# Kernel tuning notes

Hardware: AMD Instinct MI355X
Metric: run time of the kernel (lower is better)

The kernel has to match this reference:

```python
import jax, jax.numpy as jnp
import numpy as np

N_NODES = 20000
N_EDGES = 320000
NFEAT = 128
NHID = 64
NCLASS = 16
HEADS = 4
NLAYERS = 3
DT = 1.0
EPS = 1e-5
NEG_SLOPE = 0.2
# softplus(1.0) for Ks, omega, zeta (raw values all 1.0, non-learnable)
SP1 = float(np.log1p(np.exp(1.0)))


def rms_norm(x):
    rms = jnp.sqrt(jnp.mean(x * x, axis=-1, keepdims=True) + EPS)
    return x / rms


def gat_conv(x, src, dst, W_gat, att_src, att_dst, b_gat):
    # x: [N, NHID] -> per-head projections h: [N, H, NHID]
    h = (x @ W_gat).reshape(N_NODES, HEADS, NHID)
    a_src = jnp.sum(h * att_src[None], axis=-1)  # [N, H]
    a_dst = jnp.sum(h * att_dst[None], axis=-1)  # [N, H]
    e = jax.nn.leaky_relu(a_src[src] + a_dst[dst], NEG_SLOPE)  # [E, H]
    # segment softmax over incoming edges of each destination node
    e_max = jax.ops.segment_max(e, dst, num_segments=N_NODES)
    e_max = jnp.where(jnp.isfinite(e_max), e_max, 0.0)
    ex = jnp.exp(e - e_max[dst])
    denom = jax.ops.segment_sum(ex, dst, num_segments=N_NODES)
    alpha = ex / (denom[dst] + 1e-16)  # [E, H]
    msg = h[src] * alpha[:, :, None]  # [E, H, NHID]
    out = jax.ops.segment_sum(msg, dst, num_segments=N_NODES)  # [N, H, NHID]
    return out.reshape(N_NODES, HEADS * NHID) + b_gat


def setup_inputs() -> dict:
    key = jax.random.key(0)
    ks = jax.random.split(key, 10)
    s = 0.05
    x = jax.random.normal(ks[0], (N_NODES, NFEAT), dtype=jnp.float32)
    edge_index = jax.random.randint(ks[1], (2, N_EDGES), 0, N_NODES, dtype=jnp.int64)
    return {
        "x": x,
        "edge_index": edge_index,
        "W_enc": jax.random.normal(ks[2], (NFEAT, NHID), dtype=jnp.float32) * s,
        "b_enc": jnp.zeros((NHID,), dtype=jnp.float32),
        "W_gat": jax.random.normal(ks[3], (NHID, HEADS * NHID), dtype=jnp.float32) * s,
        "att_src": jax.random.normal(ks[4], (HEADS, NHID), dtype=jnp.float32) * s,
        "att_dst": jax.random.normal(ks[5], (HEADS, NHID), dtype=jnp.float32) * s,
        "b_gat": jnp.zeros((HEADS * NHID,), dtype=jnp.float32),
        "W_dec": jax.random.normal(ks[6], (NHID, NCLASS), dtype=jnp.float32) * s,
        "b_dec": jnp.zeros((NCLASS,), dtype=jnp.float32),
    }


def reference(x, edge_index, W_enc, b_enc, W_gat, att_src, att_dst, b_gat, W_dec, b_dec):
    # eval mode: dropout is identity
    Ks, omega, zeta = SP1, SP1, SP1
    omega_sq = omega * omega
    # PyG GATConv add_self_loops=True
    loops = jnp.arange(N_NODES, dtype=edge_index.dtype)
    src = jnp.concatenate([edge_index[0], loops])
    dst = jnp.concatenate([edge_index[1], loops])

    Y = jax.nn.relu(x @ W_enc + b_enc)
    X = Y
    for _ in range(NLAYERS):
        conv = jax.nn.elu(gat_conv(X, src, dst, W_gat, att_src, att_dst, b_gat))
        # faithful to original: view(N, -1, heads).mean(-1) on [N, heads*nhid]
        agg = conv.reshape(N_NODES, NHID, HEADS).mean(axis=-1)
        Y = Y + DT * (Ks * agg - 2.0 * zeta * omega * Y - omega_sq * X)
        X = X + DT * Y
        X = rms_norm(X)
        Y = rms_norm(Y)
    return X @ W_dec + b_dec
```

## Files before the change

kernel.cpp:

```cpp
#include <hip/hip_runtime.h>
#include <hip/hip_bf16.h>

#define DEV static __device__ __forceinline__

constexpr int N_NODES = 20000;
constexpr int N_EDGES = 320000;
constexpr int NFEAT = 128;
constexpr int NHID = 64;
constexpr int NCLASS = 16;
constexpr int HEADS = 4;
constexpr int HD = HEADS * NHID;
constexpr float EPSV = 1e-5f;
constexpr float SLOPE = 0.2f;
constexpr float SP1 = 1.3132616875182228f;

typedef __attribute__((ext_vector_type(8))) short short8;
typedef __attribute__((ext_vector_type(4))) float float4v;

DEV float bf2f(__hip_bfloat16 v) { return __bfloat162float(v); }
DEV short f2bfbits(float v) { return (short)__bfloat16_as_ushort(__float2bfloat16(v)); }
DEV float lrelu(float v) { return v > 0.f ? v : SLOPE * v; }
DEV int clampn(int v) { return min(max(v, 0), N_NODES - 1); }

DEV float ldf(const void* p, int i, int f32) {
  return f32 ? ((const float*)p)[i] : bf2f(((const __hip_bfloat16*)p)[i]);
}
DEV int eload(const int* e32, int is64, int idx) {
  if (is64) return (int)(((const long long*)e32)[idx]);
  return e32[idx];
}

DEV float wsum(float v) {
#pragma unroll
  for (int m = 32; m > 0; m >>= 1) v += __shfl_xor(v, m, 64);
  return v;
}
DEV float qsum(float v) {
#pragma unroll
  for (int m = 1; m < 16; m <<= 1) v += __shfl_xor(v, m, 64);
  return v;
}
DEV void acc8_i8(float* acc, int lo, int hi, float a) {
  acc[0] = fmaf((float)(signed char)(lo), a, acc[0]);
  acc[1] = fmaf((float)(signed char)(lo >> 8), a, acc[1]);
  acc[2] = fmaf((float)(signed char)(lo >> 16), a, acc[2]);
  acc[3] = fmaf((float)(lo >> 24), a, acc[3]);
  acc[4] = fmaf((float)(signed char)(hi), a, acc[4]);
  acc[5] = fmaf((float)(signed char)(hi >> 8), a, acc[5]);
  acc[6] = fmaf((float)(signed char)(hi >> 16), a, acc[6]);
  acc[7] = fmaf((float)(hi >> 24), a, acc[7]);
}

__global__ __launch_bounds__(256) void k_detect_pack(const int* __restrict__ edge,
                                                     const unsigned* __restrict__ xw,
                                                     const void* __restrict__ W_enc,
                                                     const void* __restrict__ W_gat,
                                                     int* __restrict__ flag,
                                                     short* __restrict__ packE,
                                                     short* __restrict__ packG) {
  __shared__ int sflag[2];
  int tid = threadIdx.x;
  if (tid < 64) {
    int v = edge[2 * tid + 1];
    unsigned long long nz = __ballot(v != 0);
    int bad = 0;
#pragma unroll
    for (int j = 0; j < 4; ++j) {
      unsigned w = xw[tid * 4 + j];
      unsigned ex = ((w & 0xFFFFu) >> 7) & 0xFFu;
      if (ex >= 0x90u) bad = 1;
    }
    unsigned long long anybad = __ballot(bad != 0);
    if (tid == 0) {
      sflag[0] = (nz == 0ULL) ? 1 : 0;
      sflag[1] = (anybad != 0ULL) ? 1 : 0;
      flag[0] = sflag[0];
      flag[1] = sflag[1];
    }
  }
  __syncthreads();
  int f32 = sflag[1];
  int wv = tid >> 6, lane = tid & 63;
  int quad = lane >> 4, m16 = lane & 15;
#pragma unroll
  for (int ks = 0; ks < 4; ++ks)
#pragma unroll
    for (int j = 0; j < 8; ++j)
      packE[(ks * 256 + tid) * 8 + j] =
          f2bfbits(ldf(W_enc, (ks * 32 + quad * 8 + j) * NHID + wv * 16 + m16, f32));
#pragma unroll
  for (int t = 0; t < 4; ++t)
#pragma unroll
    for (int ks = 0; ks < 2; ++ks)
#pragma unroll
      for (int j = 0; j < 8; ++j)
        packG[((t * 2 + ks) * 256 + tid) * 8 + j] =
            f2bfbits(ldf(W_gat, (ks * 32 + quad * 8 + j) * HD + wv * 64 + t * 16 + m16, f32));
}

__global__ void k_hist(const int* __restrict__ edge, const int* __restrict__ flag,
                       int* __restrict__ counts) {
  int e = blockIdx.x * blockDim.x + threadIdx.x;
  if (e < N_EDGES) {
    int d = clampn(eload(edge, flag[0], N_EDGES + e));
    atomicAdd(&counts[d], 1);
  }
}

__global__ __launch_bounds__(1024) void k_scan(const int* __restrict__ counts,
                                               int* __restrict__ rowptr,
                                               int* __restrict__ cursor) {
  __shared__ int part[1024];
  int t = threadIdx.x;
  const int CH = (N_NODES + 1023) / 1024;
  int b = t * CH, e = min(b + CH, N_NODES);
  int s = 0;
  for (int i = b; i < e; ++i) s += counts[i];
  part[t] = s;
  __syncthreads();
  for (int off = 1; off < 1024; off <<= 1) {
    int v = (t >= off) ? part[t - off] : 0;
    __syncthreads();
    part[t] += v;
    __syncthreads();
  }
  int run = (t == 0) ? 0 : part[t - 1];
  for (int i = b; i < e; ++i) {
    rowptr[i] = run;
    cursor[i] = run;
    run += counts[i];
  }
  if (t == 1023) rowptr[N_NODES] = N_EDGES;
}

__global__ void k_scatter(const int* __restrict__ edge, const int* __restrict__ flag,
                          int* __restrict__ cursor, int* __restrict__ ssort) {
  int e = blockIdx.x * blockDim.x + threadIdx.x;
  if (e < N_EDGES) {
    int is64 = flag[0];
    int s = clampn(eload(edge, is64, e));
    int d = clampn(eload(edge, is64, N_EDGES + e));
    int pos = atomicAdd(&cursor[d], 1);
    if (pos >= 0 && pos < N_EDGES) ssort[pos] = s;
  }
}

__global__ __launch_bounds__(256) void k_encoder(const void* __restrict__ x,
                                                 const short* __restrict__ packE,
                                                 const void* __restrict__ b_enc,
                                                 const int* __restrict__ flag,
                                                 float* __restrict__ X, float* __restrict__ Y) {
  int f32 = flag[1];
  int tid = threadIdx.x;
  int wv = tid >> 6, lane = tid & 63;
  int quad = lane >> 4, m16 = lane & 15;
  int n0 = blockIdx.x * 16;
  int c0 = wv * 16;

  float4v acc = {0.f, 0.f, 0.f, 0.f};
#pragma unroll
  for (int ks = 0; ks < 4; ++ks) {
    short8 bfrag = *(const short8*)(packE + (ks * 256 + tid) * 8);
    short8 afrag;
    size_t xoff = (size_t)(n0 + m16) * NFEAT + ks * 32 + quad * 8;
    if (f32) {
      float4 f0 = *(const float4*)((const float*)x + xoff);
      float4 f1 = *(const float4*)((const float*)x + xoff + 4);
      afrag[0] = f2bfbits(f0.x); afrag[1] = f2bfbits(f0.y);
      afrag[2] = f2bfbits(f0.z); afrag[3] = f2bfbits(f0.w);
      afrag[4] = f2bfbits(f1.x); afrag[5] = f2bfbits(f1.y);
      afrag[6] = f2bfbits(f1.z); afrag[7] = f2bfbits(f1.w);
    } else {
      afrag = *(const short8*)((const short*)x + xoff);
    }
    acc = __builtin_amdgcn_mfma_f32_16x16x32_bf16(afrag, bfrag, acc, 0, 0, 0);
  }

  float bias = ldf(b_enc, c0 + m16, f32);
#pragma unroll
  for (int r = 0; r < 4; ++r) {
    int n = n0 + quad * 4 + r;
    float yv = fmaxf(acc[r] + bias, 0.f);
    size_t idx = (size_t)n * NHID + c0 + m16;
    X[idx] = yv;
    Y[idx] = yv;
  }
}

__global__ __launch_bounds__(256) void k_proj(const float* __restrict__ X,
                                              const short* __restrict__ packG,
                                              const void* __restrict__ att_src,
                                              const void* __restrict__ att_dst,
                                              const int* __restrict__ flag,
                                              signed char* __restrict__ hb,
                                              float* __restrict__ nodeinfo,
                                              float* __restrict__ a_dst) {
  __shared__ float smax[4][16];
  int f32 = flag[1];
  int tid = threadIdx.x;
  int wv = tid >> 6, lane = tid & 63;
  int quad = lane >> 4, m16 = lane & 15;
  int n0 = blockIdx.x * 16;

  short8 afrag[2];
#pragma unroll
  for (int ks = 0; ks < 2; ++ks) {
    size_t xoff = (size_t)(n0 + m16) * NHID + ks * 32 + quad * 8;
    float4 f0 = *(const float4*)(X + xoff);
    float4 f1 = *(const float4*)(X + xoff + 4);
    afrag[ks][0] = f2bfbits(f0.x); afrag[ks][1] = f2bfbits(f0.y);
    afrag[ks][2] = f2bfbits(f0.z); afrag[ks][3] = f2bfbits(f0.w);
    afrag[ks][4] = f2bfbits(f1.x); afrag[ks][5] = f2bfbits(f1.y);
    afrag[ks][6] = f2bfbits(f1.z); afrag[ks][7] = f2bfbits(f1.w);
  }

  float4v acc[4];
#pragma unroll
  for (int t = 0; t < 4; ++t) {
    acc[t] = (float4v){0.f, 0.f, 0.f, 0.f};
#pragma unroll
    for (int ks = 0; ks < 2; ++ks) {
      short8 bfrag = *(const short8*)(packG + ((t * 2 + ks) * 256 + tid) * 8);
      acc[t] = __builtin_amdgcn_mfma_f32_16x16x32_bf16(afrag[ks], bfrag, acc[t], 0, 0, 0);
    }
  }

  float amax[4];
#pragma unroll
  for (int r = 0; r < 4; ++r) {
    float m = fmaxf(fmaxf(fabsf(acc[0][r]), fabsf(acc[1][r])),
                    fmaxf(fabsf(acc[2][r]), fabsf(acc[3][r])));
#pragma unroll
    for (int sh = 1; sh < 16; sh <<= 1) m = fmaxf(m, __shfl_xor(m, sh, 64));
    amax[r] = m;
  }
  if (m16 == 0) {
#pragma unroll
    for (int r = 0; r < 4; ++r) smax[wv][quad * 4 + r] = amax[r];
  }
  __syncthreads();
  float inv[4], rmax[4];
#pragma unroll
  for (int r = 0; r < 4; ++r) {
    int row = quad * 4 + r;
    float m = fmaxf(fmaxf(smax[0][row], smax[1][row]), fmaxf(smax[2][row], smax[3][row]));
    rmax[r] = m;
    inv[r] = (m > 0.f) ? 127.f / m : 0.f;
  }

  float avs[4], avd[4];
#pragma unroll
  for (int t = 0; t < 4; ++t) {
    avs[t] = ldf(att_src, wv * 64 + t * 16 + m16, f32);
    avd[t] = ldf(att_dst, wv * 64 + t * 16 + m16, f32);
  }
  float ps[4], pd[4];
#pragma unroll
  for (int r = 0; r < 4; ++r) { ps[r] = 0.f; pd[r] = 0.f; }
#pragma unroll
  for (int t = 0; t < 4; ++t) {
#pragma unroll
    for (int r = 0; r < 4; ++r) {
      int n = n0 + quad * 4 + r;
      hb[(size_t)n * HD + wv * 64 + t * 16 + m16] =
          (signed char)__float2int_rn(acc[t][r] * inv[r]);
      ps[r] = fmaf(acc[t][r], avs[t], ps[r]);
      pd[r] = fmaf(acc[t][r], avd[t], pd[r]);
    }
  }
#pragma unroll
  for (int r = 0; r < 4; ++r) {
    float s = qsum(ps[r]);
    float dq = qsum(pd[r]);
    if (m16 == 0) {
      int n = n0 + quad * 4 + r;
      nodeinfo[(size_t)n * 8 + wv * 2] = s;
      nodeinfo[(size_t)n * 8 + wv * 2 + 1] = rmax[r] * (1.f / 127.f);
      a_dst[n * HEADS + wv] = dq;
    }
  }
}

__global__ __launch_bounds__(256) void k_layer(const signed char* __restrict__ hb,
                                               const float* __restrict__ nodeinfo,
                                               const float* __restrict__ a_dst,
                                               const int* __restrict__ rowptr,
                                               const int* __restrict__ srcs,
                                               const void* __restrict__ b_gat,
                                               const int* __restrict__ flag,
                                               float* __restrict__ X, float* __restrict__ Y) {
  int wave = threadIdx.x >> 6, lane = threadIdx.x & 63;
  int half = lane >> 5, l32 = lane & 31, head = l32 >> 3;
  int f32 = flag[1];
  int d = blockIdx.x * 4 + wave;
  if (d >= N_NODES) return;
  int beg = rowptr[d];
  int end = rowptr[d + 1];
  beg = min(max(beg, 0), N_EDGES);
  end = min(max(end, beg), N_EDGES);
  float advh = a_dst[d * 4 + head];

  float acc[8];
#pragma unroll
  for (int k = 0; k < 8; ++k) acc[k] = 0.f;
  float sw = 0.f;

  {
    float2 nid = *(const float2*)(nodeinfo + (size_t)d * 8 + head * 2);
    float wself = __expf(lrelu(nid.x + advh));
    if (half == 0) {
      sw = wself;
      uint2 hv = *(const uint2*)(hb + (size_t)d * HD + l32 * 8);
      acc8_i8(acc, (int)hv.x, (int)hv.y, wself * nid.y);
    }
  }
  int p = beg;
  for (; p + 8 <= end; p += 8) {
    int q0 = p + half, q1 = p + 2 + half, q2 = p + 4 + half, q3 = p + 6 + half;
    int s0 = clampn(srcs[q0]), s1 = clampn(srcs[q1]);
    int s2 = clampn(srcs[q2]), s3 = clampn(srcs[q3]);
    float2 n0v = *(const float2*)(nodeinfo + (size_t)s0 * 8 + head * 2);
    float2 n1v = *(const float2*)(nodeinfo + (size_t)s1 * 8 + head * 2);
    float2 n2v = *(const float2*)(nodeinfo + (size_t)s2 * 8 + head * 2);
    float2 n3v = *(const float2*)(nodeinfo + (size_t)s3 * 8 + head * 2);
    uint2 h0 = *(const uint2*)(hb + (size_t)s0 * HD + l32 * 8);
    uint2 h1 = *(const uint2*)(hb + (size_t)s1 * HD + l32 * 8);
    uint2 h2 = *(const uint2*)(hb + (size_t)s2 * HD + l32 * 8);
    uint2 h3 = *(const uint2*)(hb + (size_t)s3 * HD + l32 * 8);
    float w0 = __expf(lrelu(n0v.x + advh));
    float w1 = __expf(lrelu(n1v.x + advh));
    float w2 = __expf(lrelu(n2v.x + advh));
    float w3 = __expf(lrelu(n3v.x + advh));
    sw += w0 + w1 + w2 + w3;
    acc8_i8(acc, (int)h0.x, (int)h0.y, w0 * n0v.y);
    acc8_i8(acc, (int)h1.x, (int)h1.y, w1 * n1v.y);
    acc8_i8(acc, (int)h2.x, (int)h2.y, w2 * n2v.y);
    acc8_i8(acc, (int)h3.x, (int)h3.y, w3 * n3v.y);
  }
  for (; p < end; p += 2) {
    int q = p + half;
    bool act = q < end;
    int s = clampn(srcs[act ? q : end - 1]);
    float2 nv = *(const float2*)(nodeinfo + (size_t)s * 8 + head * 2);
    uint2 hv = *(const uint2*)(hb + (size_t)s * HD + l32 * 8);
    float w = act ? __expf(lrelu(nv.x + advh)) : 0.f;
    sw += w;
    acc8_i8(acc, (int)hv.x, (int)hv.y, w * nv.y);
  }
  sw += __shfl_xor(sw, 32, 64);
#pragma unroll
  for (int k = 0; k < 8; ++k) acc[k] += __shfl_xor(acc[k], 32, 64);
  float invh = 1.f / (sw + 1e-16f);

  float cg[8];
#pragma unroll
  for (int k = 0; k < 8; ++k) {
    float c = acc[k] * invh + ldf(b_gat, l32 * 8 + k, f32);
    cg[k] = c > 0.f ? c : expm1f(c);
  }
  float agg0 = 0.25f * (cg[0] + cg[1] + cg[2] + cg[3]);
  float agg1 = 0.25f * (cg[4] + cg[5] + cg[6] + cg[7]);

  size_t ix = (size_t)d * NHID + l32 * 2;
  float xv0 = X[ix], xv1 = X[ix + 1];
  float yv0 = Y[ix], yv1 = Y[ix + 1];
  float yn0 = yv0 + (SP1 * agg0 - 2.f * SP1 * SP1 * yv0 - SP1 * SP1 * xv0);
  float yn1 = yv1 + (SP1 * agg1 - 2.f * SP1 * SP1 * yv1 - SP1 * SP1 * xv1);
  float xn0 = xv0 + yn0;
  float xn1 = xv1 + yn1;

  float msx = wsum(xn0 * xn0 + xn1 * xn1) * (1.f / 128.f);
  float rx = rsqrtf(msx + EPSV);
  float msy = wsum(yn0 * yn0 + yn1 * yn1) * (1.f / 128.f);
  float ry = rsqrtf(msy + EPSV);
  X[ix] = xn0 * rx; X[ix + 1] = xn1 * rx;
  Y[ix] = yn0 * ry; Y[ix + 1] = yn1 * ry;
}

__global__ __launch_bounds__(256) void k_dec(const float* __restrict__ X,
                                             const void* __restrict__ W_dec,
                                             const void* __restrict__ b_dec,
                                             const int* __restrict__ flag,
                                             float* __restrict__ out) {
  __shared__ float Wl[NHID * NCLASS];
  __shared__ float bl[NCLASS];
  int f32 = flag[1];
  int tid = threadIdx.x;
  for (int i = tid; i < NHID * NCLASS; i += 256) Wl[i] = ldf(W_dec, i, f32);
  if (tid < NCLASS) bl[tid] = ldf(b_dec, tid, f32);
  __syncthreads();
  int g = blockIdx.x * 256 + tid;
  if (g >= N_NODES * NCLASS) return;
  int n = g >> 4, c = g & 15;
  const float* xr = X + (size_t)n * NHID;
  float acc = bl[c];
#pragma unroll
  for (int k = 0; k < NHID; ++k) acc = fmaf(xr[k], Wl[k * NCLASS + c], acc);
  if (!(acc == acc) || fabsf(acc) > 1e6f) acc = 777.0f;
  out[g] = acc;
}

extern "C" void kernel_launch(void* const* d_in, const int* in_sizes, int n_in,
                              void* d_out, int out_size, void* d_ws, size_t ws_size,
                              hipStream_t stream) {
  const void* x       = d_in[0];
  const int*  edge    = (const int*)d_in[1];
  const void* W_enc   = d_in[2];
  const void* b_enc   = d_in[3];
  const void* W_gat   = d_in[4];
  const void* att_src = d_in[5];
  const void* att_dst = d_in[6];
  const void* b_gat   = d_in[7];
  const void* W_dec   = d_in[8];
  const void* b_dec   = d_in[9];

  char* ws = (char*)d_ws;
  size_t off = 0;
  auto alloc = [&](size_t bytes) -> void* {
    if (off + bytes > ws_size) off = 0;
    void* p = ws + off;
    off = (off + bytes + 255) & ~(size_t)255;
    return p;
  };
  int*   flag    = (int*)alloc(256);
  int*   counts  = (int*)alloc((size_t)N_NODES * 4);
  int*   rowptr  = (int*)alloc((size_t)(N_NODES + 1) * 4);
  int*   cursor  = (int*)alloc((size_t)N_NODES * 4);
  int*   ssort   = (int*)alloc((size_t)N_EDGES * 4);
  float* nodeinfo= (float*)alloc((size_t)N_NODES * 8 * 4);
  float* a_dst   = (float*)alloc((size_t)N_NODES * HEADS * 4);
  float* X       = (float*)alloc((size_t)N_NODES * NHID * 4);
  float* Y       = (float*)alloc((size_t)N_NODES * NHID * 4);
  short* packE   = (short*)alloc((size_t)4 * 256 * 8 * 2);
  short* packG   = (short*)alloc((size_t)8 * 256 * 8 * 2);
  signed char* hb = (signed char*)alloc((size_t)N_NODES * HD);

  hipMemsetAsync(counts, 0, (size_t)N_NODES * 4, stream);
  k_detect_pack<<<1, 256, 0, stream>>>(edge, (const unsigned*)x, W_enc, W_gat, flag, packE, packG);
  k_hist<<<(N_EDGES + 255) / 256, 256, 0, stream>>>(edge, flag, counts);
  k_scan<<<1, 1024, 0, stream>>>(counts, rowptr, cursor);
  k_scatter<<<(N_EDGES + 255) / 256, 256, 0, stream>>>(edge, flag, cursor, ssort);

  k_encoder<<<N_NODES / 16, 256, 0, stream>>>(x, packE, b_enc, flag, X, Y);
  for (int l = 0; l < 3; ++l) {
    k_proj<<<N_NODES / 16, 256, 0, stream>>>(X, packG, att_src, att_dst, flag, hb, nodeinfo, a_dst);
    k_layer<<<N_NODES / 4, 256, 0, stream>>>(hb, nodeinfo, a_dst, rowptr, ssort, b_gat, flag, X, Y);
  }
  k_dec<<<(N_NODES * NCLASS + 255) / 256, 256, 0, stream>>>(X, W_dec, b_dec, flag, (float*)d_out);
}
```

Before: 334.0 us.

## Gather 16 int8 features per lane and process four edges per wave step

```diff
diff --git a/kernel.cpp b/kernel.cpp
--- a/kernel.cpp
+++ b/kernel.cpp
@@ -40,15 +40,17 @@
   for (int m = 1; m < 16; m <<= 1) v += __shfl_xor(v, m, 64);
   return v;
 }
-DEV void acc8_i8(float* acc, int lo, int hi, float a) {
-  acc[0] = fmaf((float)(signed char)(lo), a, acc[0]);
-  acc[1] = fmaf((float)(signed char)(lo >> 8), a, acc[1]);
-  acc[2] = fmaf((float)(signed char)(lo >> 16), a, acc[2]);
-  acc[3] = fmaf((float)(lo >> 24), a, acc[3]);
-  acc[4] = fmaf((float)(signed char)(hi), a, acc[4]);
-  acc[5] = fmaf((float)(signed char)(hi >> 8), a, acc[5]);
-  acc[6] = fmaf((float)(signed char)(hi >> 16), a, acc[6]);
-  acc[7] = fmaf((float)(hi >> 24), a, acc[7]);
+DEV void acc4_i8(float* acc, int w, float a) {
+  acc[0] = fmaf((float)(signed char)(w), a, acc[0]);
+  acc[1] = fmaf((float)(signed char)(w >> 8), a, acc[1]);
+  acc[2] = fmaf((float)(signed char)(w >> 16), a, acc[2]);
+  acc[3] = fmaf((float)(w >> 24), a, acc[3]);
+}
+DEV void acc16_i8(float* acc, uint4 hv, float a) {
+  acc4_i8(acc + 0, (int)hv.x, a);
+  acc4_i8(acc + 4, (int)hv.y, a);
+  acc4_i8(acc + 8, (int)hv.z, a);
+  acc4_i8(acc + 12, (int)hv.w, a);
 }
 
 __global__ __launch_bounds__(256) void k_detect_pack(const int* __restrict__ edge,
@@ -290,7 +292,7 @@
                                                const int* __restrict__ flag,
                                                float* __restrict__ X, float* __restrict__ Y) {
   int wave = threadIdx.x >> 6, lane = threadIdx.x & 63;
-  int half = lane >> 5, l32 = lane & 31, head = l32 >> 3;
+  int qtr = lane >> 4, l16 = lane & 15, head = l16 >> 2;
   int f32 = flag[1];
   int d = blockIdx.x * 4 + wave;
   if (d >= N_NODES) return;
@@ -300,81 +302,82 @@
   end = min(max(end, beg), N_EDGES);
   float advh = a_dst[d * 4 + head];
 
-  float acc[8];
-#pragma unroll
-  for (int k = 0; k < 8; ++k) acc[k] = 0.f;
+  float acc[16];
+#pragma unroll
+  for (int k = 0; k < 16; ++k) acc[k] = 0.f;
   float sw = 0.f;
 
   {
-    float2 nid = *(const float2*)(nodeinfo + (size_t)d * 8 + head * 2);
+    float2 nid = *(const float2*)(nodeinfo + ((unsigned)d << 3) + head * 2);
     float wself = __expf(lrelu(nid.x + advh));
-    if (half == 0) {
+    if (qtr == 0) {
       sw = wself;
-      uint2 hv = *(const uint2*)(hb + (size_t)d * HD + l32 * 8);
-      acc8_i8(acc, (int)hv.x, (int)hv.y, wself * nid.y);
+      uint4 hv = *(const uint4*)(hb + ((unsigned)d << 8) + (l16 << 4));
+      acc16_i8(acc, hv, wself * nid.y);
     }
   }
   int p = beg;
   for (; p + 8 <= end; p += 8) {
-    int q0 = p + half, q1 = p + 2 + half, q2 = p + 4 + half, q3 = p + 6 + half;
-    int s0 = clampn(srcs[q0]), s1 = clampn(srcs[q1]);
-    int s2 = clampn(srcs[q2]), s3 = clampn(srcs[q3]);
-    float2 n0v = *(const float2*)(nodeinfo + (size_t)s0 * 8 + head * 2);
-    float2 n1v = *(const float2*)(nodeinfo + (size_t)s1 * 8 + head * 2);
-    float2 n2v = *(const float2*)(nodeinfo + (size_t)s2 * 8 + head * 2);
-    float2 n3v = *(const float2*)(nodeinfo + (size_t)s3 * 8 + head * 2);
-    uint2 h0 = *(const uint2*)(hb + (size_t)s0 * HD + l32 * 8);
-    uint2 h1 = *(const uint2*)(hb + (size_t)s1 * HD + l32 * 8);
-    uint2 h2 = *(const uint2*)(hb + (size_t)s2 * HD + l32 * 8);
-    uint2 h3 = *(const uint2*)(hb + (size_t)s3 * HD + l32 * 8);
+    int q0 = p + qtr, q1 = p + 4 + qtr;
+    int s0 = srcs[q0], s1 = srcs[q1];
+    float2 n0v = *(const float2*)(nodeinfo + ((unsigned)s0 << 3) + head * 2);
+    float2 n1v = *(const float2*)(nodeinfo + ((unsigned)s1 << 3) + head * 2);
+    uint4 h0 = *(const uint4*)(hb + ((unsigned)s0 << 8) + (l16 << 4));
+    uint4 h1 = *(const uint4*)(hb + ((unsigned)s1 << 8) + (l16 << 4));
     float w0 = __expf(lrelu(n0v.x + advh));
     float w1 = __expf(lrelu(n1v.x + advh));
-    float w2 = __expf(lrelu(n2v.x + advh));
-    float w3 = __expf(lrelu(n3v.x + advh));
-    sw += w0 + w1 + w2 + w3;
-    acc8_i8(acc, (int)h0.x, (int)h0.y, w0 * n0v.y);
-    acc8_i8(acc, (int)h1.x, (int)h1.y, w1 * n1v.y);
-    acc8_i8(acc, (int)h2.x, (int)h2.y, w2 * n2v.y);
-    acc8_i8(acc, (int)h3.x, (int)h3.y, w3 * n3v.y);
-  }
-  for (; p < end; p += 2) {
-    int q = p + half;
+    sw += w0 + w1;
+    acc16_i8(acc, h0, w0 * n0v.y);
+    acc16_i8(acc, h1, w1 * n1v.y);
+  }
+  for (; p < end; p += 4) {
+    int q = p + qtr;
     bool act = q < end;
-    int s = clampn(srcs[act ? q : end - 1]);
-    float2 nv = *(const float2*)(nodeinfo + (size_t)s * 8 + head * 2);
-    uint2 hv = *(const uint2*)(hb + (size_t)s * HD + l32 * 8);
+    int s = act ? srcs[q] : d;
+    float2 nv = *(const float2*)(nodeinfo + ((unsigned)s << 3) + head * 2);
+    uint4 hv = *(const uint4*)(hb + ((unsigned)s << 8) + (l16 << 4));
     float w = act ? __expf(lrelu(nv.x + advh)) : 0.f;
     sw += w;
-    acc8_i8(acc, (int)hv.x, (int)hv.y, w * nv.y);
-  }
+    acc16_i8(acc, hv, w * nv.y);
+  }
+  sw += __shfl_xor(sw, 16, 64);
   sw += __shfl_xor(sw, 32, 64);
 #pragma unroll
-  for (int k = 0; k < 8; ++k) acc[k] += __shfl_xor(acc[k], 32, 64);
+  for (int k = 0; k < 16; ++k) {
+    acc[k] += __shfl_xor(acc[k], 16, 64);
+    acc[k] += __shfl_xor(acc[k], 32, 64);
+  }
   float invh = 1.f / (sw + 1e-16f);
 
-  float cg[8];
-#pragma unroll
-  for (int k = 0; k < 8; ++k) {
-    float c = acc[k] * invh + ldf(b_gat, l32 * 8 + k, f32);
+  float cg[16];
+#pragma unroll
+  for (int k = 0; k < 16; ++k) {
+    float c = acc[k] * invh + ldf(b_gat, l16 * 16 + k, f32);
     cg[k] = c > 0.f ? c : expm1f(c);
   }
-  float agg0 = 0.25f * (cg[0] + cg[1] + cg[2] + cg[3]);
-  float agg1 = 0.25f * (cg[4] + cg[5] + cg[6] + cg[7]);
-
-  size_t ix = (size_t)d * NHID + l32 * 2;
-  float xv0 = X[ix], xv1 = X[ix + 1];
-  float yv0 = Y[ix], yv1 = Y[ix + 1];
-  float yn0 = yv0 + (SP1 * agg0 - 2.f * SP1 * SP1 * yv0 - SP1 * SP1 * xv0);
-  float yn1 = yv1 + (SP1 * agg1 - 2.f * SP1 * SP1 * yv1 - SP1 * SP1 * xv1);
-  float xn0 = xv0 + yn0;
-  float xn1 = xv1 + yn1;
-
-  float msx = wsum(xn0 * xn0 + xn1 * xn1) * (1.f / 128.f);
+  float agg[4];
+#pragma unroll
+  for (int g = 0; g < 4; ++g)
+    agg[g] = 0.25f * (cg[g * 4] + cg[g * 4 + 1] + cg[g * 4 + 2] + cg[g * 4 + 3]);
+
+  size_t ix = (size_t)d * NHID + l16 * 4;
+  float4 xv = *(const float4*)(X + ix);
+  float4 yv = *(const float4*)(Y + ix);
+  float yn[4], xn[4];
+  float xvv[4] = {xv.x, xv.y, xv.z, xv.w};
+  float yvv[4] = {yv.x, yv.y, yv.z, yv.w};
+#pragma unroll
+  for (int g = 0; g < 4; ++g) {
+    yn[g] = yvv[g] + (SP1 * agg[g] - 2.f * SP1 * SP1 * yvv[g] - SP1 * SP1 * xvv[g]);
+    xn[g] = xvv[g] + yn[g];
+  }
+
+  float msx = wsum(xn[0] * xn[0] + xn[1] * xn[1] + xn[2] * xn[2] + xn[3] * xn[3]) * (1.f / 256.f);
   float rx = rsqrtf(msx + EPSV);
-  float msy = wsum(yn0 * yn0 + yn1 * yn1) * (1.f / 128.f);
+  float msy = wsum(yn[0] * yn[0] + yn[1] * yn[1] + yn[2] * yn[2] + yn[3] * yn[3]) * (1.f / 256.f);
   float ry = rsqrtf(msy + EPSV);
-  X[ix] = xn0 * rx; X[ix + 1] = xn1 * rx;
-  Y[ix] = yn0 * ry; Y[ix + 1] = yn1 * ry;
+  *(float4*)(X + ix) = make_float4(xn[0] * rx, xn[1] * rx, xn[2] * rx, xn[3] * rx);
+  *(float4*)(Y + ix) = make_float4(yn[0] * ry, yn[1] * ry, yn[2] * ry, yn[3] * ry);
 }
 
 __global__ __launch_bounds__(256) void k_dec(const float* __restrict__ X,
```

Measured after the change: 392.7 us. +17.6%, slower.

## Merge setup kernels and fuse decoder into last GAT layer

Applied to the files above, without the earlier changes.

```diff
diff --git a/kernel.cpp b/kernel.cpp
--- a/kernel.cpp
+++ b/kernel.cpp
@@ -51,15 +51,28 @@
   acc[7] = fmaf((float)(hi >> 24), a, acc[7]);
 }
 
-__global__ __launch_bounds__(256) void k_detect_pack(const int* __restrict__ edge,
-                                                     const unsigned* __restrict__ xw,
-                                                     const void* __restrict__ W_enc,
-                                                     const void* __restrict__ W_gat,
-                                                     int* __restrict__ flag,
-                                                     short* __restrict__ packE,
-                                                     short* __restrict__ packG) {
+__global__ __launch_bounds__(256) void k_histpack(const int* __restrict__ edge,
+                                                  const unsigned* __restrict__ xw,
+                                                  const void* __restrict__ W_enc,
+                                                  const void* __restrict__ W_gat,
+                                                  int* __restrict__ flag,
+                                                  short* __restrict__ packE,
+                                                  short* __restrict__ packG,
+                                                  int* __restrict__ counts) {
+  int b = blockIdx.x;
+  int tid = threadIdx.x;
+  if (b < 1250) {
+    int lane = tid & 63;
+    int v = edge[2 * lane + 1];
+    int is64 = (__ballot(v != 0) == 0ULL) ? 1 : 0;
+    int e = b * 256 + tid;
+    if (e < N_EDGES) {
+      int d = clampn(eload(edge, is64, N_EDGES + e));
+      atomicAdd(&counts[d], 1);
+    }
+    return;
+  }
   __shared__ int sflag[2];
-  int tid = threadIdx.x;
   if (tid < 64) {
     int v = edge[2 * tid + 1];
     unsigned long long nz = __ballot(v != 0);
@@ -96,15 +109,6 @@
       for (int j = 0; j < 8; ++j)
         packG[((t * 2 + ks) * 256 + tid) * 8 + j] =
             f2bfbits(ldf(W_gat, (ks * 32 + quad * 8 + j) * HD + wv * 64 + t * 16 + m16, f32));
-}
-
-__global__ void k_hist(const int* __restrict__ edge, const int* __restrict__ flag,
-                       int* __restrict__ counts) {
-  int e = blockIdx.x * blockDim.x + threadIdx.x;
-  if (e < N_EDGES) {
-    int d = clampn(eload(edge, flag[0], N_EDGES + e));
-    atomicAdd(&counts[d], 1);
-  }
 }
 
 __global__ __launch_bounds__(1024) void k_scan(const int* __restrict__ counts,
@@ -133,28 +137,32 @@
   if (t == 1023) rowptr[N_NODES] = N_EDGES;
 }
 
-__global__ void k_scatter(const int* __restrict__ edge, const int* __restrict__ flag,
-                          int* __restrict__ cursor, int* __restrict__ ssort) {
-  int e = blockIdx.x * blockDim.x + threadIdx.x;
-  if (e < N_EDGES) {
-    int is64 = flag[0];
-    int s = clampn(eload(edge, is64, e));
-    int d = clampn(eload(edge, is64, N_EDGES + e));
-    int pos = atomicAdd(&cursor[d], 1);
-    if (pos >= 0 && pos < N_EDGES) ssort[pos] = s;
-  }
-}
-
-__global__ __launch_bounds__(256) void k_encoder(const void* __restrict__ x,
-                                                 const short* __restrict__ packE,
-                                                 const void* __restrict__ b_enc,
-                                                 const int* __restrict__ flag,
-                                                 float* __restrict__ X, float* __restrict__ Y) {
+__global__ __launch_bounds__(256) void k_encscatter(const void* __restrict__ x,
+                                                    const short* __restrict__ packE,
+                                                    const void* __restrict__ b_enc,
+                                                    const int* __restrict__ edge,
+                                                    const int* __restrict__ flag,
+                                                    int* __restrict__ cursor,
+                                                    int* __restrict__ ssort,
+                                                    float* __restrict__ X,
+                                                    float* __restrict__ Y) {
+  int blk = blockIdx.x;
+  int tid = threadIdx.x;
+  if (blk >= 1250) {
+    int e = (blk - 1250) * 256 + tid;
+    if (e < N_EDGES) {
+      int is64 = flag[0];
+      int s = clampn(eload(edge, is64, e));
+      int d = clampn(eload(edge, is64, N_EDGES + e));
+      int pos = atomicAdd(&cursor[d], 1);
+      if (pos >= 0 && pos < N_EDGES) ssort[pos] = s;
+    }
+    return;
+  }
   int f32 = flag[1];
-  int tid = threadIdx.x;
   int wv = tid >> 6, lane = tid & 63;
   int quad = lane >> 4, m16 = lane & 15;
-  int n0 = blockIdx.x * 16;
+  int n0 = blk * 16;
   int c0 = wv * 16;
 
   float4v acc = {0.f, 0.f, 0.f, 0.f};
@@ -288,12 +296,15 @@
                                                const int* __restrict__ srcs,
                                                const void* __restrict__ b_gat,
                                                const int* __restrict__ flag,
-                                               float* __restrict__ X, float* __restrict__ Y) {
+                                               float* __restrict__ X, float* __restrict__ Y,
+                                               const void* __restrict__ W_dec,
+                                               const void* __restrict__ b_dec,
+                                               float* __restrict__ out) {
+  __shared__ float xl[4 * NHID];
   int wave = threadIdx.x >> 6, lane = threadIdx.x & 63;
   int half = lane >> 5, l32 = lane & 31, head = l32 >> 3;
   int f32 = flag[1];
   int d = blockIdx.x * 4 + wave;
-  if (d >= N_NODES) return;
   int beg = rowptr[d];
   int end = rowptr[d + 1];
   beg = min(max(beg, 0), N_EDGES);
@@ -306,27 +317,27 @@
   float sw = 0.f;
 
   {
-    float2 nid = *(const float2*)(nodeinfo + (size_t)d * 8 + head * 2);
+    float2 nid = *(const float2*)(nodeinfo + ((unsigned)d << 3) + head * 2);
     float wself = __expf(lrelu(nid.x + advh));
     if (half == 0) {
       sw = wself;
-      uint2 hv = *(const uint2*)(hb + (size_t)d * HD + l32 * 8);
+      uint2 hv = *(const uint2*)(hb + ((unsigned)d << 8) + (l32 << 3));
       acc8_i8(acc, (int)hv.x, (int)hv.y, wself * nid.y);
     }
   }
   int p = beg;
   for (; p + 8 <= end; p += 8) {
     int q0 = p + half, q1 = p + 2 + half, q2 = p + 4 + half, q3 = p + 6 + half;
-    int s0 = clampn(srcs[q0]), s1 = clampn(srcs[q1]);
-    int s2 = clampn(srcs[q2]), s3 = clampn(srcs[q3]);
-    float2 n0v = *(const float2*)(nodeinfo + (size_t)s0 * 8 + head * 2);
-    float2 n1v = *(const float2*)(nodeinfo + (size_t)s1 * 8 + head * 2);
-    float2 n2v = *(const float2*)(nodeinfo + (size_t)s2 * 8 + head * 2);
-    float2 n3v = *(const float2*)(nodeinfo + (size_t)s3 * 8 + head * 2);
-    uint2 h0 = *(const uint2*)(hb + (size_t)s0 * HD + l32 * 8);
-    uint2 h1 = *(const uint2*)(hb + (size_t)s1 * HD + l32 * 8);
-    uint2 h2 = *(const uint2*)(hb + (size_t)s2 * HD + l32 * 8);
-    uint2 h3 = *(const uint2*)(hb + (size_t)s3 * HD + l32 * 8);
+    int s0 = srcs[q0], s1 = srcs[q1];
+    int s2 = srcs[q2], s3 = srcs[q3];
+    float2 n0v = *(const float2*)(nodeinfo + ((unsigned)s0 << 3) + head * 2);
+    float2 n1v = *(const float2*)(nodeinfo + ((unsigned)s1 << 3) + head * 2);
+    float2 n2v = *(const float2*)(nodeinfo + ((unsigned)s2 << 3) + head * 2);
+    float2 n3v = *(const float2*)(nodeinfo + ((unsigned)s3 << 3) + head * 2);
+    uint2 h0 = *(const uint2*)(hb + ((unsigned)s0 << 8) + (l32 << 3));
+    uint2 h1 = *(const uint2*)(hb + ((unsigned)s1 << 8) + (l32 << 3));
+    uint2 h2 = *(const uint2*)(hb + ((unsigned)s2 << 8) + (l32 << 3));
+    uint2 h3 = *(const uint2*)(hb + ((unsigned)s3 << 8) + (l32 << 3));
     float w0 = __expf(lrelu(n0v.x + advh));
     float w1 = __expf(lrelu(n1v.x + advh));
     float w2 = __expf(lrelu(n2v.x + advh));
@@ -340,9 +351,9 @@
   for (; p < end; p += 2) {
     int q = p + half;
     bool act = q < end;
-    int s = clampn(srcs[act ? q : end - 1]);
-    float2 nv = *(const float2*)(nodeinfo + (size_t)s * 8 + head * 2);
-    uint2 hv = *(const uint2*)(hb + (size_t)s * HD + l32 * 8);
+    int s = act ? srcs[q] : d;
+    float2 nv = *(const float2*)(nodeinfo + ((unsigned)s << 3) + head * 2);
+    uint2 hv = *(const uint2*)(hb + ((unsigned)s << 8) + (l32 << 3));
     float w = act ? __expf(lrelu(nv.x + advh)) : 0.f;
     sw += w;
     acc8_i8(acc, (int)hv.x, (int)hv.y, w * nv.y);
@@ -373,31 +384,27 @@
   float rx = rsqrtf(msx + EPSV);
   float msy = wsum(yn0 * yn0 + yn1 * yn1) * (1.f / 128.f);
   float ry = rsqrtf(msy + EPSV);
-  X[ix] = xn0 * rx; X[ix + 1] = xn1 * rx;
+  float fx0 = xn0 * rx, fx1 = xn1 * rx;
+  X[ix] = fx0; X[ix + 1] = fx1;
   Y[ix] = yn0 * ry; Y[ix + 1] = yn1 * ry;
-}
-
-__global__ __launch_bounds__(256) void k_dec(const float* __restrict__ X,
-                                             const void* __restrict__ W_dec,
-                                             const void* __restrict__ b_dec,
-                                             const int* __restrict__ flag,
-                                             float* __restrict__ out) {
-  __shared__ float Wl[NHID * NCLASS];
-  __shared__ float bl[NCLASS];
-  int f32 = flag[1];
-  int tid = threadIdx.x;
-  for (int i = tid; i < NHID * NCLASS; i += 256) Wl[i] = ldf(W_dec, i, f32);
-  if (tid < NCLASS) bl[tid] = ldf(b_dec, tid, f32);
-  __syncthreads();
-  int g = blockIdx.x * 256 + tid;
-  if (g >= N_NODES * NCLASS) return;
-  int n = g >> 4, c = g & 15;
-  const float* xr = X + (size_t)n * NHID;
-  float acc = bl[c];
-#pragma unroll
-  for (int k = 0; k < NHID; ++k) acc = fmaf(xr[k], Wl[k * NCLASS + c], acc);
-  if (!(acc == acc) || fabsf(acc) > 1e6f) acc = 777.0f;
-  out[g] = acc;
+
+  if (out != nullptr) {
+    if (half == 0) {
+      xl[wave * NHID + l32 * 2] = fx0;
+      xl[wave * NHID + l32 * 2 + 1] = fx1;
+    }
+    __syncthreads();
+    if (lane < NCLASS) {
+      int c = lane;
+      float a = ldf(b_dec, c, f32);
+      const float* xr = xl + wave * NHID;
+#pragma unroll
+      for (int k = 0; k < NHID; ++k)
+        a = fmaf(xr[k], ldf(W_dec, k * NCLASS + c, f32), a);
+      if (!(a == a) || fabsf(a) > 1e6f) a = 777.0f;
+      out[d * NCLASS + c] = a;
+    }
+  }
 }
 
 extern "C" void kernel_launch(void* const* d_in, const int* in_sizes, int n_in,
@@ -436,15 +443,16 @@
   signed char* hb = (signed char*)alloc((size_t)N_NODES * HD);
 
   hipMemsetAsync(counts, 0, (size_t)N_NODES * 4, stream);
-  k_detect_pack<<<1, 256, 0, stream>>>(edge, (const unsigned*)x, W_enc, W_gat, flag, packE, packG);
-  k_hist<<<(N_EDGES + 255) / 256, 256, 0, stream>>>(edge, flag, counts);
+  k_histpack<<<1251, 256, 0, stream>>>(edge, (const unsigned*)x, W_enc, W_gat,
+                                       flag, packE, packG, counts);
   k_scan<<<1, 1024, 0, stream>>>(counts, rowptr, cursor);
-  k_scatter<<<(N_EDGES + 255) / 256, 256, 0, stream>>>(edge, flag, cursor, ssort);
-
-  k_encoder<<<N_NODES / 16, 256, 0, stream>>>(x, packE, b_enc, flag, X, Y);
+  k_encscatter<<<2500, 256, 0, stream>>>(x, packE, b_enc, edge, flag, cursor, ssort, X, Y);
+
   for (int l = 0; l < 3; ++l) {
-    k_proj<<<N_NODES / 16, 256, 0, stream>>>(X, packG, att_src, att_dst, flag, hb, nodeinfo, a_dst);
-    k_layer<<<N_NODES / 4, 256, 0, stream>>>(hb, nodeinfo, a_dst, rowptr, ssort, b_gat, flag, X, Y);
-  }
-  k_dec<<<(N_NODES * NCLASS + 255) / 256, 256, 0, stream>>>(X, W_dec, b_dec, flag, (float*)d_out);
-}
+    k_proj<<<N_NODES / 16, 256, 0, stream>>>(X, packG, att_src, att_dst, flag,
+                                             hb, nodeinfo, a_dst);
+    float* outp = (l == 2) ? (float*)d_out : nullptr;
+    k_layer<<<N_NODES / 4, 256, 0, stream>>>(hb, nodeinfo, a_dst, rowptr, ssort, b_gat,
+                                             flag, X, Y, W_dec, b_dec, outp);
+  }
+}
```

After: 387.6 us. +16.1%, slower.
